# Kernel tuning notes

Measured on AMD Instinct MI355X. Metric: run time of the kernel, lower is better.

Reference implementation:

```python
import jax, jax.numpy as jnp
import numpy as np

E = 384        # number of edges
HID = 128      # hidden_dim
NH = 8         # num_heads
DH = HID // NH # head_dim = 16
NR = 64        # num_radial
CUTOFF = 10.0
AIN = 2 * DH + NR + 1  # attention MLP input dim = 97


def _xavier(key, fan_in, fan_out):
    a = np.sqrt(6.0 / (fan_in + fan_out))
    return jax.random.uniform(key, (fan_in, fan_out), jnp.float32, -a, a)


def setup_inputs() -> dict:
    key = jax.random.key(0)
    ks = jax.random.split(key, 16)
    return {
        "edge_features": jax.random.normal(ks[0], (E, HID), jnp.float32),
        "edge_coords": jax.random.normal(ks[1], (E, 3), jnp.float32),
        "edge_mask": jnp.zeros((E, E), jnp.float32),  # 0 = connected
        "wq": _xavier(ks[2], HID, HID),
        "wk": _xavier(ks[3], HID, HID),
        "wv": _xavier(ks[4], HID, HID),
        "rbf_centers": jnp.linspace(0.0, CUTOFF, NR).astype(jnp.float32),
        "rbf_widths": jnp.full((NR,), 0.5, jnp.float32),
        "a_w1": _xavier(ks[5], AIN, HID), "a_b1": jnp.zeros((HID,), jnp.float32),
        "a_w2": _xavier(ks[6], HID, HID), "a_b2": jnp.zeros((HID,), jnp.float32),
        "a_w3": _xavier(ks[7], HID, NH),  "a_b3": jnp.zeros((NH,), jnp.float32),
        "g_w1": _xavier(ks[8], DH, HID),  "g_b1": jnp.zeros((HID,), jnp.float32),
        "g_w2": _xavier(ks[9], HID, 1),   "g_b2": jnp.zeros((1,), jnp.float32),
        "wo": _xavier(ks[10], HID, HID),  "bo": jnp.zeros((HID,), jnp.float32),
        "ln_g": jnp.ones((HID,), jnp.float32),
        "ln_b": jnp.zeros((HID,), jnp.float32),
        "edge_index": jax.random.randint(ks[11], (2, E), 0, E, jnp.int64) if jax.config.jax_enable_x64 else jax.random.randint(ks[11], (2, E), 0, E, jnp.int32),
    }


def reference(edge_features, edge_coords, edge_mask,
              wq, wk, wv, rbf_centers, rbf_widths,
              a_w1, a_b1, a_w2, a_b2, a_w3, a_b3,
              g_w1, g_b1, g_w2, g_b2, wo, bo, ln_g, ln_b,
              edge_index):
    silu = jax.nn.silu
    n = edge_features.shape[0]

    q = (edge_features @ wq).reshape(n, NH, DH)
    k = (edge_features @ wk).reshape(n, NH, DH)
    v = (edge_features @ wv).reshape(n, NH, DH)

    # pairwise geometry [E, E, ...]
    coord_diff = edge_coords[:, None, :] - edge_coords[None, :, :]
    dist = jnp.linalg.norm(coord_diff, axis=-1) + 1e-8
    dist = jnp.clip(dist, 1e-8, 1e8)
    dot = jnp.clip(jnp.sum(edge_coords[:, None, :] * edge_coords[None, :, :], -1),
                   -1e8, 1e8)
    d = dist[..., None]                               # [E, E, 1]
    rbf = jnp.exp(-rbf_widths * (d - rbf_centers) ** 2) * (d <= CUTOFF).astype(jnp.float32)

    feats = []
    coords = edge_coords
    for h in range(NH):  # structural loop over fixed num_heads
        qh = jnp.broadcast_to(q[:, h, None, :], (n, n, DH))
        kh = jnp.broadcast_to(k[None, :, h, :], (n, n, DH))
        ai = jnp.concatenate([qh, kh, rbf, dot[..., None]], -1)  # [E, E, 97]
        x = silu(ai @ a_w1 + a_b1)
        x = silu(x @ a_w2 + a_b2)
        scores = (x @ a_w3 + a_b3)[:, :, h] + edge_mask
        scores = jnp.clip(scores, -1e9, 1e9)
        attn = jax.nn.softmax(scores, axis=-1)
        attn = jnp.nan_to_num(attn, nan=0.0, posinf=1.0, neginf=0.0)
        vh = v[:, h, :]
        feats.append(attn @ vh)
        # coord gate from v_head of the query edge, broadcast over keys
        gates = jax.nn.sigmoid(silu(vh @ g_w1 + g_b1) @ g_w2 + g_b2)  # [E, 1]
        coords = coords + jnp.einsum('ij,ijc->ic', attn * gates, coord_diff) / NH

    upd = jnp.concatenate(feats, -1)             # [E, hidden]
    y = edge_features + upd @ wo + bo            # residual + out_proj
    mu = jnp.mean(y, -1, keepdims=True)
    var = jnp.var(y, -1, keepdims=True)
    out_f = (y - mu) / jnp.sqrt(var + 1e-5) * ln_g + ln_b
    return out_f, coords
```

## Files before the change

kernel.cpp:

```cpp
#include <hip/hip_runtime.h>
#include <hip/hip_bf16.h>

#define N 384
#define HIDN 128
#define NHD 8
#define DHD 16
#define NRB 64
#define CUTF 10.0f

#define WS_V 0
#define WS_QPB (WS_V + N*HIDN)
#define WS_KPB (WS_QPB + N*NHD*HIDN/2)
#define WS_GATE (WS_KPB + N*NHD*HIDN/2)
#define WS_UPD (WS_GATE + N*NHD)
#define WS_SCORES (WS_UPD + N*HIDN)
#define WS_W2BF (WS_SCORES + NHD*N*N)

typedef short bf16x8 __attribute__((ext_vector_type(8)));
typedef float floatx4 __attribute__((ext_vector_type(4)));
#define MFMA16(a, b, c) __builtin_amdgcn_mfma_f32_16x16x32_bf16(a, b, c, 0, 0, 0)

__device__ __forceinline__ float siluf(float x) { return x / (1.0f + __expf(-x)); }
__device__ __forceinline__ float silu_fast(float x) {
    return x * __builtin_amdgcn_rcpf(1.0f + __expf(-x));
}
__device__ __forceinline__ short f2bf(float f) {
    unsigned int b = __float_as_uint(f);
    unsigned int r = (b + 0x7fffu + ((b >> 16) & 1u)) >> 16;
    return (short)r;
}
__device__ __forceinline__ float bf2f(short s) {
    return __uint_as_float(((unsigned int)(unsigned short)s) << 16);
}
__device__ __forceinline__ unsigned int cvt_pk_bf16(float lo, float hi) {
    unsigned int r;
    asm("v_cvt_pk_bf16_f32 %0, %1, %2" : "=v"(r) : "v"(lo), "v"(hi));
    return r;
}
__device__ __forceinline__ float wave_sum(float v) {
    for (int o = 32; o; o >>= 1) v += __shfl_down(v, o, 64);
    return v;
}

__global__ __launch_bounds__(128) void k_pre(const float* __restrict__ ef,
    const float* __restrict__ wq, const float* __restrict__ wk, const float* __restrict__ wv,
    const float* __restrict__ aw1, const float* __restrict__ aw2,
    const float* __restrict__ gw1, const float* __restrict__ gb1,
    const float* __restrict__ gw2, const float* __restrict__ gb2,
    float* __restrict__ v, unsigned short* __restrict__ Qpb,
    unsigned short* __restrict__ Kpb, float* __restrict__ gates,
    unsigned short* __restrict__ w2bf) {
    __shared__ float sE[HIDN], sQ[HIDN], sK[HIDN], sV[HIDN];
    __shared__ float sG[NHD][2];
    int i = blockIdx.x, t = threadIdx.x;
    if (i < HIDN) w2bf[(size_t)i * HIDN + t] = (unsigned short)f2bf(aw2[t * HIDN + i]);
    sE[t] = ef[i * HIDN + t];
    __syncthreads();
    float aq = 0.f, ak = 0.f, av = 0.f;
#pragma unroll 8
    for (int c = 0; c < HIDN; c++) {
        float e = sE[c];
        aq += e * wq[c * HIDN + t];
        ak += e * wk[c * HIDN + t];
        av += e * wv[c * HIDN + t];
    }
    v[i * HIDN + t] = av;
    sQ[t] = aq; sK[t] = ak; sV[t] = av;
    __syncthreads();
    for (int h = 0; h < NHD; h++) {
        float accq = 0.f, acck = 0.f;
#pragma unroll
        for (int d = 0; d < DHD; d++) {
            accq += sQ[h * DHD + d] * aw1[d * HIDN + t];
            acck += sK[h * DHD + d] * aw1[(DHD + d) * HIDN + t];
        }
        Qpb[((size_t)h * N + i) * HIDN + t] = (unsigned short)f2bf(accq);
        Kpb[((size_t)h * N + i) * HIDN + t] = (unsigned short)f2bf(acck);
        float tt = gb1[t];
#pragma unroll
        for (int d = 0; d < DHD; d++) tt += sV[h * DHD + d] * gw1[d * HIDN + t];
        float contrib = siluf(tt) * gw2[t];
        float s = wave_sum(contrib);
        if ((t & 63) == 0) sG[h][t >> 6] = s;
    }
    __syncthreads();
    if (t < NHD)
        gates[i * NHD + t] = 1.0f / (1.0f + __expf(-(sG[t][0] + sG[t][1] + gb2[0])));
}

#define OFF_W2T  0
#define OFF_QPB  32768
#define OFF_SDD  34816
#define OFF_RBF  34944
#define OFF_R    39040
#define OFF_B2W3 47488
#define SMEM_SZ  52096

__global__ __launch_bounds__(512, 4) void k_scores_mfma(
    const float* __restrict__ coords, const float* __restrict__ mask,
    const float* __restrict__ centers, const float* __restrict__ widths,
    const float* __restrict__ aw1, const float* __restrict__ ab1,
    const float* __restrict__ ab2,
    const float* __restrict__ aw3, const float* __restrict__ ab3,
    const unsigned short* __restrict__ Qpb, const unsigned short* __restrict__ Kpb,
    const unsigned short* __restrict__ w2bf,
    float* __restrict__ scores) {
    __shared__ __align__(16) char smem[SMEM_SZ];
    const int t = threadIdx.x;
    const int lane = t & 63;
    const int w = t >> 6;
    const int l15 = lane & 15;
    const int quad = lane >> 4;
    const int i = blockIdx.y;
    const int jb = blockIdx.x * 96;

    {
        const uint4* src = (const uint4*)w2bf;
        for (int idx = t; idx < 2048; idx += 512) {
            int row = idx >> 4, slot = idx & 15;
            *(uint4*)(smem + OFF_W2T + row * 256 + ((slot * 16) ^ ((row & 7) << 4))) = src[idx];
        }
    }
    if (t < 128)
        ((uint4*)(smem + OFF_QPB))[t] = ((const uint4*)(Qpb + (size_t)i * NHD * HIDN))[t];
    for (int idx = t; idx < HIDN * NHD; idx += 512) {
        int c = idx >> 3, h = idx & 7;
        unsigned int lo = (unsigned short)f2bf(ab2[c]);
        unsigned int hi = (unsigned short)f2bf(aw3[c * NHD + h]);
        *(unsigned int*)(smem + OFF_B2W3 + (c * 9 + h) * 4) = (hi << 16) | lo;
    }
    const int c0 = w * 16 + l15;
    bf16x8 BW1[2];
#pragma unroll
    for (int ks = 0; ks < 2; ks++) {
        bf16x8 a;
#pragma unroll
        for (int e = 0; e < 8; e++) {
            int r = ks * 32 + quad * 8 + e;
            a[e] = f2bf(aw1[(32 + r) * HIDN + c0]);
        }
        BW1[ks] = a;
    }
    const float b1v = ab1[c0];
    const float w1dv = aw1[96 * HIDN + c0];
    const float ab3v = ab3[w];
    const float cr = centers[lane], rwd = widths[lane];
    const float cix = coords[i * 3], ciy = coords[i * 3 + 1], ciz = coords[i * 3 + 2];
    __syncthreads();

    for (int ch = 0; ch < 3; ch++) {
        const int j0 = jb + ch * 32;
        {
#pragma unroll
            for (int p = 0; p < 4; p++) {
                int j = w + p * 8;
                int jj = j0 + j;
                float jx = coords[jj * 3], jy = coords[jj * 3 + 1], jz = coords[jj * 3 + 2];
                float dx = cix - jx, dy = ciy - jy, dz = ciz - jz;
                float dist = sqrtf(dx * dx + dy * dy + dz * dz) + 1e-8f;
                dist = fminf(fmaxf(dist, 1e-8f), 1e8f);
                float dd = dist - cr;
                float val = (dist <= CUTF) ? __expf(-rwd * dd * dd) : 0.0f;
                *(short*)(smem + OFF_RBF + j * 128 + ((lane * 2) ^ ((j & 7) << 4))) = f2bf(val);
            }
            if (t < 32) {
                int jj = j0 + t;
                float jx = coords[jj * 3], jy = coords[jj * 3 + 1], jz = coords[jj * 3 + 2];
                float dot = fminf(fmaxf(cix * jx + ciy * jy + ciz * jz, -1e8f), 1e8f);
                *(float*)(smem + OFF_SDD + t * 4) = dot;
            }
        }
        __syncthreads();
#pragma unroll
        for (int jt = 0; jt < 2; jt++) {
            {
                int jl = jt * 16 + l15;
                int sw = (jl & 7) << 4;
                bf16x8 ra0 = *(const bf16x8*)(smem + OFF_RBF + jl * 128 + ((quad * 16) ^ sw));
                bf16x8 ra1 = *(const bf16x8*)(smem + OFF_RBF + jl * 128 + ((64 + quad * 16) ^ sw));
                floatx4 acc;
#pragma unroll
                for (int r = 0; r < 4; r++) {
                    float dotv = *(const float*)(smem + OFF_SDD + (jt * 16 + quad * 4 + r) * 4);
                    acc[r] = b1v + dotv * w1dv;
                }
                acc = MFMA16(ra0, BW1[0], acc);
                acc = MFMA16(ra1, BW1[1], acc);
#pragma unroll
                for (int r = 0; r < 4; r++)
                    *(float*)(smem + OFF_R + (quad * 4 + r) * 528 + c0 * 4) = acc[r];
            }
            __syncthreads();
            {
                const int jr = j0 + jt * 16 + l15;
                bf16x8 A[4];
#pragma unroll
                for (int f = 0; f < 4; f++) {
                    const int c8 = f * 32 + quad * 8;
                    bf16x8 kp = *(const bf16x8*)(Kpb + ((size_t)w * N + jr) * HIDN + c8);
                    bf16x8 qp = *(const bf16x8*)(smem + OFF_QPB + (w * HIDN + c8) * 2);
                    const char* rbase = smem + OFF_R + l15 * 528 + c8 * 4;
                    float4 r0 = *(const float4*)(rbase);
                    float4 r1 = *(const float4*)(rbase + 16);
                    float xs[8] = {r0.x, r0.y, r0.z, r0.w, r1.x, r1.y, r1.z, r1.w};
                    union { unsigned int u[4]; bf16x8 v; } uu;
#pragma unroll
                    for (int e2 = 0; e2 < 4; e2++) {
                        float xa = silu_fast(bf2f(kp[2 * e2])     + bf2f(qp[2 * e2])     + xs[2 * e2]);
                        float xb = silu_fast(bf2f(kp[2 * e2 + 1]) + bf2f(qp[2 * e2 + 1]) + xs[2 * e2 + 1]);
                        uu.u[e2] = cvt_pk_bf16(xa, xb);
                    }
                    A[f] = uu.v;
                }
                float part[4] = {0.f, 0.f, 0.f, 0.f};
#pragma unroll 2
                for (int ct = 0; ct < 8; ct++) {
                    const int rw2 = ct * 16 + l15;
                    const char* wb = smem + OFF_W2T + rw2 * 256;
                    const int sw = (rw2 & 7) << 4;
                    bf16x8 b0 = *(const bf16x8*)(wb + ((quad * 16) ^ sw));
                    bf16x8 b1 = *(const bf16x8*)(wb + ((64 + quad * 16) ^ sw));
                    bf16x8 b2 = *(const bf16x8*)(wb + ((128 + quad * 16) ^ sw));
                    bf16x8 b3 = *(const bf16x8*)(wb + ((192 + quad * 16) ^ sw));
                    unsigned int pk = *(const unsigned int*)(smem + OFF_B2W3 + (rw2 * 9 + w) * 4);
                    float bb = bf2f((short)(pk & 0xffffu));
                    float ww = bf2f((short)(pk >> 16));
                    floatx4 acc = {bb, bb, bb, bb};
                    acc = MFMA16(A[0], b0, acc);
                    acc = MFMA16(A[1], b1, acc);
                    acc = MFMA16(A[2], b2, acc);
                    acc = MFMA16(A[3], b3, acc);
#pragma unroll
                    for (int r = 0; r < 4; r++)
                        part[r] += silu_fast(acc[r]) * ww;
                }
#pragma unroll
                for (int off = 1; off < 16; off <<= 1) {
#pragma unroll
                    for (int r = 0; r < 4; r++)
                        part[r] += __shfl_xor(part[r], off, 64);
                }
                if (l15 == 0) {
                    const int jo = j0 + jt * 16 + quad * 4;
                    float4 mv = *(const float4*)(mask + (size_t)i * N + jo);
                    float4 sv;
                    sv.x = fminf(fmaxf(part[0] + ab3v + mv.x, -1e9f), 1e9f);
                    sv.y = fminf(fmaxf(part[1] + ab3v + mv.y, -1e9f), 1e9f);
                    sv.z = fminf(fmaxf(part[2] + ab3v + mv.z, -1e9f), 1e9f);
                    sv.w = fminf(fmaxf(part[3] + ab3v + mv.w, -1e9f), 1e9f);
                    *(float4*)(scores + ((size_t)w * N + i) * N + jo) = sv;
                }
            }
            __syncthreads();
        }
    }
}

__global__ __launch_bounds__(256) void k_attn2(
    const float* __restrict__ scores, const float* __restrict__ v,
    const float* __restrict__ gates, const float* __restrict__ coords,
    const float* __restrict__ ef, const float* __restrict__ wo,
    const float* __restrict__ bo, const float* __restrict__ lng,
    const float* __restrict__ lnb, float* __restrict__ out) {
    __shared__ float sA[4][N];
    __shared__ float sCrd[N * 3];
    __shared__ float sC[NHD][3];
    __shared__ float sUpd[HIDN];
    __shared__ float sR2[2];
    int i = blockIdx.x, t = threadIdx.x, w = t >> 6, lane = t & 63;
    for (int idx = t; idx < N * 3; idx += 256) sCrd[idx] = coords[idx];
    float cix = coords[i * 3], ciy = coords[i * 3 + 1], ciz = coords[i * 3 + 2];
    __syncthreads();
    for (int hh = 0; hh < 2; hh++) {
        int h = hh * 4 + w;
        const float* srow = scores + ((size_t)h * N + i) * N;
        float s[6];
#pragma unroll
        for (int p = 0; p < 6; p++) s[p] = srow[lane + 64 * p];
        float m = s[0];
#pragma unroll
        for (int p = 1; p < 6; p++) m = fmaxf(m, s[p]);
        for (int off = 1; off < 64; off <<= 1) m = fmaxf(m, __shfl_xor(m, off, 64));
        float e[6], sum = 0.f;
#pragma unroll
        for (int p = 0; p < 6; p++) { e[p] = __expf(s[p] - m); sum += e[p]; }
        for (int off = 1; off < 64; off <<= 1) sum += __shfl_xor(sum, off, 64);
        float inv = 1.0f / sum;
#pragma unroll
        for (int p = 0; p < 6; p++) sA[w][lane + 64 * p] = e[p] * inv;
        __syncthreads();
        int d4 = lane & 3, grp = lane >> 2;
        float4 f4 = {0.f, 0.f, 0.f, 0.f};
        for (int j = grp; j < N; j += 16) {
            float a = sA[w][j];
            float4 vv = *(const float4*)(v + j * HIDN + h * DHD + d4 * 4);
            f4.x += a * vv.x; f4.y += a * vv.y; f4.z += a * vv.z; f4.w += a * vv.w;
        }
#pragma unroll
        for (int off = 4; off < 64; off <<= 1) {
            f4.x += __shfl_xor(f4.x, off, 64);
            f4.y += __shfl_xor(f4.y, off, 64);
            f4.z += __shfl_xor(f4.z, off, 64);
            f4.w += __shfl_xor(f4.w, off, 64);
        }
        if (lane < 4) *(float4*)(&sUpd[h * DHD + lane * 4]) = f4;
        float cx = 0.f, cy = 0.f, cz = 0.f;
#pragma unroll
        for (int p = 0; p < 6; p++) {
            int j = lane + 64 * p;
            float a = sA[w][j];
            cx += a * (cix - sCrd[j * 3]);
            cy += a * (ciy - sCrd[j * 3 + 1]);
            cz += a * (ciz - sCrd[j * 3 + 2]);
        }
        for (int off = 1; off < 64; off <<= 1) {
            cx += __shfl_xor(cx, off, 64);
            cy += __shfl_xor(cy, off, 64);
            cz += __shfl_xor(cz, off, 64);
        }
        if (lane == 0) {
            float g = gates[i * NHD + h] * (1.0f / NHD);
            sC[h][0] = g * cx; sC[h][1] = g * cy; sC[h][2] = g * cz;
        }
        __syncthreads();
    }
    if (t < 3) {
        float acc = coords[i * 3 + t];
#pragma unroll
        for (int h = 0; h < NHD; h++) acc += sC[h][t];
        out[N * HIDN + i * 3 + t] = acc;
    }
    int c = t & 127;
    float y = ef[i * HIDN + c] + bo[c];
#pragma unroll 8
    for (int cp = 0; cp < HIDN; cp++) y += sUpd[cp] * wo[cp * HIDN + c];
    float ssum = wave_sum(y);
    if (t < 128 && (t & 63) == 0) sR2[t >> 6] = ssum;
    __syncthreads();
    float mu = (sR2[0] + sR2[1]) * (1.0f / HIDN);
    __syncthreads();
    float dv = y - mu;
    float s2 = wave_sum(dv * dv);
    if (t < 128 && (t & 63) == 0) sR2[t >> 6] = s2;
    __syncthreads();
    float var = (sR2[0] + sR2[1]) * (1.0f / HIDN);
    if (t < 128) out[i * HIDN + c] = dv * rsqrtf(var + 1e-5f) * lng[c] + lnb[c];
}

extern "C" void kernel_launch(void* const* d_in, const int* in_sizes, int n_in,
                              void* d_out, int out_size, void* d_ws, size_t ws_size,
                              hipStream_t stream) {
    const float* ef      = (const float*)d_in[0];
    const float* coords  = (const float*)d_in[1];
    const float* mask    = (const float*)d_in[2];
    const float* wq      = (const float*)d_in[3];
    const float* wk      = (const float*)d_in[4];
    const float* wv      = (const float*)d_in[5];
    const float* centers = (const float*)d_in[6];
    const float* widths  = (const float*)d_in[7];
    const float* aw1     = (const float*)d_in[8];
    const float* ab1     = (const float*)d_in[9];
    const float* aw2     = (const float*)d_in[10];
    const float* ab2     = (const float*)d_in[11];
    const float* aw3     = (const float*)d_in[12];
    const float* ab3     = (const float*)d_in[13];
    const float* gw1     = (const float*)d_in[14];
    const float* gb1     = (const float*)d_in[15];
    const float* gw2     = (const float*)d_in[16];
    const float* gb2     = (const float*)d_in[17];
    const float* wo      = (const float*)d_in[18];
    const float* bo      = (const float*)d_in[19];
    const float* lng     = (const float*)d_in[20];
    const float* lnb     = (const float*)d_in[21];
    float* ws = (float*)d_ws;
    float* v      = ws + WS_V;
    unsigned short* Qpb = (unsigned short*)(ws + WS_QPB);
    unsigned short* Kpb = (unsigned short*)(ws + WS_KPB);
    float* gates  = ws + WS_GATE;
    float* scores = ws + WS_SCORES;
    unsigned short* w2bf = (unsigned short*)(ws + WS_W2BF);
    float* out = (float*)d_out;

    k_pre<<<N, 128, 0, stream>>>(ef, wq, wk, wv, aw1, aw2, gw1, gb1, gw2, gb2, v, Qpb, Kpb, gates, w2bf);
    k_scores_mfma<<<dim3(4, N), 512, 0, stream>>>(
        coords, mask, centers, widths, aw1, ab1, ab2, aw3, ab3, Qpb, Kpb, w2bf, scores);
    k_attn2<<<N, 256, 0, stream>>>(scores, v, gates, coords, ef, wo, bo, lng, lnb, out);
}
```

Baseline: 253.4 us.

## Software-pipeline RBF computation, store first-layer result as bf16, split out-proj across threads

Result: no change. 255.2 us (+0.7%).

```diff
diff --git a/kernel.cpp b/kernel.cpp
--- a/kernel.cpp
+++ b/kernel.cpp
@@ -93,8 +93,9 @@
 #define OFF_SDD  34816
 #define OFF_RBF  34944
 #define OFF_R    39040
-#define OFF_B2W3 47488
-#define SMEM_SZ  52096
+#define OFF_B2   47744
+#define OFF_W3T  48256
+#define SMEM_SZ  52352
 
 __global__ __launch_bounds__(512, 4) void k_scores_mfma(
     const float* __restrict__ coords, const float* __restrict__ mask,
@@ -121,13 +122,13 @@
             *(uint4*)(smem + OFF_W2T + row * 256 + ((slot * 16) ^ ((row & 7) << 4))) = src[idx];
         }
     }
-    if (t < 128)
+    if (t < 128) {
         ((uint4*)(smem + OFF_QPB))[t] = ((const uint4*)(Qpb + (size_t)i * NHD * HIDN))[t];
+        *(float*)(smem + OFF_B2 + t * 4) = ab2[t];
+    }
     for (int idx = t; idx < HIDN * NHD; idx += 512) {
-        int c = idx >> 3, h = idx & 7;
-        unsigned int lo = (unsigned short)f2bf(ab2[c]);
-        unsigned int hi = (unsigned short)f2bf(aw3[c * NHD + h]);
-        *(unsigned int*)(smem + OFF_B2W3 + (c * 9 + h) * 4) = (hi << 16) | lo;
+        int h = idx >> 7, c = idx & 127;
+        *(float*)(smem + OFF_W3T + (h * 128 + c) * 4) = aw3[c * NHD + h];
     }
     const int c0 = w * 16 + l15;
     bf16x8 BW1[2];
@@ -146,15 +147,56 @@
     const float ab3v = ab3[w];
     const float cr = centers[lane], rwd = widths[lane];
     const float cix = coords[i * 3], ciy = coords[i * 3 + 1], ciz = coords[i * 3 + 2];
+
+    {
+#pragma unroll
+        for (int p = 0; p < 4; p++) {
+            int j = w + p * 8;
+            int jj = jb + j;
+            float jx = coords[jj * 3], jy = coords[jj * 3 + 1], jz = coords[jj * 3 + 2];
+            float dx = cix - jx, dy = ciy - jy, dz = ciz - jz;
+            float dist = sqrtf(dx * dx + dy * dy + dz * dz) + 1e-8f;
+            dist = fminf(fmaxf(dist, 1e-8f), 1e8f);
+            float dd = dist - cr;
+            float val = (dist <= CUTF) ? __expf(-rwd * dd * dd) : 0.0f;
+            *(short*)(smem + OFF_RBF + j * 128 + ((lane * 2) ^ ((j & 7) << 4))) = f2bf(val);
+        }
+        if (t < 32) {
+            int jj = jb + t;
+            float jx = coords[jj * 3], jy = coords[jj * 3 + 1], jz = coords[jj * 3 + 2];
+            float dot = fminf(fmaxf(cix * jx + ciy * jy + ciz * jz, -1e8f), 1e8f);
+            *(float*)(smem + OFF_SDD + t * 4) = dot;
+        }
+    }
     __syncthreads();
 
     for (int ch = 0; ch < 3; ch++) {
         const int j0 = jb + ch * 32;
-        {
+#pragma unroll
+        for (int jt = 0; jt < 2; jt++) {
+            int jl = jt * 16 + l15;
+            int sw = (jl & 7) << 4;
+            bf16x8 ra0 = *(const bf16x8*)(smem + OFF_RBF + jl * 128 + ((quad * 16) ^ sw));
+            bf16x8 ra1 = *(const bf16x8*)(smem + OFF_RBF + jl * 128 + ((64 + quad * 16) ^ sw));
+            floatx4 acc;
+#pragma unroll
+            for (int r = 0; r < 4; r++) {
+                float dotv = *(const float*)(smem + OFF_SDD + (jt * 16 + quad * 4 + r) * 4);
+                acc[r] = b1v + dotv * w1dv;
+            }
+            acc = MFMA16(ra0, BW1[0], acc);
+            acc = MFMA16(ra1, BW1[1], acc);
+#pragma unroll
+            for (int r = 0; r < 4; r++)
+                *(short*)(smem + OFF_R + (jt * 16 + quad * 4 + r) * 272 + c0 * 2) = f2bf(acc[r]);
+        }
+        __syncthreads();
+        if (ch < 2) {
+            const int j0n = j0 + 32;
 #pragma unroll
             for (int p = 0; p < 4; p++) {
                 int j = w + p * 8;
-                int jj = j0 + j;
+                int jj = j0n + j;
                 float jx = coords[jj * 3], jy = coords[jj * 3 + 1], jz = coords[jj * 3 + 2];
                 float dx = cix - jx, dy = ciy - jy, dz = ciz - jz;
                 float dist = sqrtf(dx * dx + dy * dy + dz * dz) + 1e-8f;
@@ -164,95 +206,70 @@
                 *(short*)(smem + OFF_RBF + j * 128 + ((lane * 2) ^ ((j & 7) << 4))) = f2bf(val);
             }
             if (t < 32) {
-                int jj = j0 + t;
+                int jj = j0n + t;
                 float jx = coords[jj * 3], jy = coords[jj * 3 + 1], jz = coords[jj * 3 + 2];
                 float dot = fminf(fmaxf(cix * jx + ciy * jy + ciz * jz, -1e8f), 1e8f);
                 *(float*)(smem + OFF_SDD + t * 4) = dot;
             }
         }
+#pragma unroll
+        for (int jt = 0; jt < 2; jt++) {
+            const int jl = jt * 16 + l15;
+            bf16x8 A[4];
+#pragma unroll
+            for (int f = 0; f < 4; f++) {
+                const int c8 = f * 32 + quad * 8;
+                bf16x8 kp = *(const bf16x8*)(Kpb + ((size_t)w * N + j0 + jl) * HIDN + c8);
+                bf16x8 qp = *(const bf16x8*)(smem + OFF_QPB + (w * HIDN + c8) * 2);
+                bf16x8 rr = *(const bf16x8*)(smem + OFF_R + (jt * 16 + l15) * 272 + c8 * 2);
+                union { unsigned int u[4]; bf16x8 v; } uu;
+#pragma unroll
+                for (int e2 = 0; e2 < 4; e2++) {
+                    float xa = silu_fast(bf2f(kp[2 * e2])     + bf2f(qp[2 * e2])     + bf2f(rr[2 * e2]));
+                    float xb = silu_fast(bf2f(kp[2 * e2 + 1]) + bf2f(qp[2 * e2 + 1]) + bf2f(rr[2 * e2 + 1]));
+                    uu.u[e2] = cvt_pk_bf16(xa, xb);
+                }
+                A[f] = uu.v;
+            }
+            float part[4] = {0.f, 0.f, 0.f, 0.f};
+#pragma unroll 2
+            for (int ct = 0; ct < 8; ct++) {
+                const int rw2 = ct * 16 + l15;
+                const char* wb = smem + OFF_W2T + rw2 * 256;
+                const int sw = (rw2 & 7) << 4;
+                bf16x8 b0 = *(const bf16x8*)(wb + ((quad * 16) ^ sw));
+                bf16x8 b1 = *(const bf16x8*)(wb + ((64 + quad * 16) ^ sw));
+                bf16x8 b2 = *(const bf16x8*)(wb + ((128 + quad * 16) ^ sw));
+                bf16x8 b3 = *(const bf16x8*)(wb + ((192 + quad * 16) ^ sw));
+                float bb = *(const float*)(smem + OFF_B2 + rw2 * 4);
+                float ww = *(const float*)(smem + OFF_W3T + (w * 128 + rw2) * 4);
+                floatx4 acc = {bb, bb, bb, bb};
+                acc = MFMA16(A[0], b0, acc);
+                acc = MFMA16(A[1], b1, acc);
+                acc = MFMA16(A[2], b2, acc);
+                acc = MFMA16(A[3], b3, acc);
+#pragma unroll
+                for (int r = 0; r < 4; r++)
+                    part[r] += silu_fast(acc[r]) * ww;
+            }
+#pragma unroll
+            for (int off = 1; off < 16; off <<= 1) {
+#pragma unroll
+                for (int r = 0; r < 4; r++)
+                    part[r] += __shfl_xor(part[r], off, 64);
+            }
+            if (l15 == 0) {
+                const int jo = j0 + jt * 16 + quad * 4;
+                float4 mv = *(const float4*)(mask + (size_t)i * N + jo);
+                float4 sv;
+                sv.x = fminf(fmaxf(part[0] + ab3v + mv.x, -1e9f), 1e9f);
+                sv.y = fminf(fmaxf(part[1] + ab3v + mv.y, -1e9f), 1e9f);
+                sv.z = fminf(fmaxf(part[2] + ab3v + mv.z, -1e9f), 1e9f);
+                sv.w = fminf(fmaxf(part[3] + ab3v + mv.w, -1e9f), 1e9f);
+                *(float4*)(scores + ((size_t)w * N + i) * N + jo) = sv;
+            }
+        }
         __syncthreads();
-#pragma unroll
-        for (int jt = 0; jt < 2; jt++) {
-            {
-                int jl = jt * 16 + l15;
-                int sw = (jl & 7) << 4;
-                bf16x8 ra0 = *(const bf16x8*)(smem + OFF_RBF + jl * 128 + ((quad * 16) ^ sw));
-                bf16x8 ra1 = *(const bf16x8*)(smem + OFF_RBF + jl * 128 + ((64 + quad * 16) ^ sw));
-                floatx4 acc;
-#pragma unroll
-                for (int r = 0; r < 4; r++) {
-                    float dotv = *(const float*)(smem + OFF_SDD + (jt * 16 + quad * 4 + r) * 4);
-                    acc[r] = b1v + dotv * w1dv;
-                }
-                acc = MFMA16(ra0, BW1[0], acc);
-                acc = MFMA16(ra1, BW1[1], acc);
-#pragma unroll
-                for (int r = 0; r < 4; r++)
-                    *(float*)(smem + OFF_R + (quad * 4 + r) * 528 + c0 * 4) = acc[r];
-            }
-            __syncthreads();
-            {
-                const int jr = j0 + jt * 16 + l15;
-                bf16x8 A[4];
-#pragma unroll
-                for (int f = 0; f < 4; f++) {
-                    const int c8 = f * 32 + quad * 8;
-                    bf16x8 kp = *(const bf16x8*)(Kpb + ((size_t)w * N + jr) * HIDN + c8);
-                    bf16x8 qp = *(const bf16x8*)(smem + OFF_QPB + (w * HIDN + c8) * 2);
-                    const char* rbase = smem + OFF_R + l15 * 528 + c8 * 4;
-                    float4 r0 = *(const float4*)(rbase);
-                    float4 r1 = *(const float4*)(rbase + 16);
-                    float xs[8] = {r0.x, r0.y, r0.z, r0.w, r1.x, r1.y, r1.z, r1.w};
-                    union { unsigned int u[4]; bf16x8 v; } uu;
-#pragma unroll
-                    for (int e2 = 0; e2 < 4; e2++) {
-                        float xa = silu_fast(bf2f(kp[2 * e2])     + bf2f(qp[2 * e2])     + xs[2 * e2]);
-                        float xb = silu_fast(bf2f(kp[2 * e2 + 1]) + bf2f(qp[2 * e2 + 1]) + xs[2 * e2 + 1]);
-                        uu.u[e2] = cvt_pk_bf16(xa, xb);
-                    }
-                    A[f] = uu.v;
-                }
-                float part[4] = {0.f, 0.f, 0.f, 0.f};
-#pragma unroll 2
-                for (int ct = 0; ct < 8; ct++) {
-                    const int rw2 = ct * 16 + l15;
-                    const char* wb = smem + OFF_W2T + rw2 * 256;
-                    const int sw = (rw2 & 7) << 4;
-                    bf16x8 b0 = *(const bf16x8*)(wb + ((quad * 16) ^ sw));
-                    bf16x8 b1 = *(const bf16x8*)(wb + ((64 + quad * 16) ^ sw));
-                    bf16x8 b2 = *(const bf16x8*)(wb + ((128 + quad * 16) ^ sw));
-                    bf16x8 b3 = *(const bf16x8*)(wb + ((192 + quad * 16) ^ sw));
-                    unsigned int pk = *(const unsigned int*)(smem + OFF_B2W3 + (rw2 * 9 + w) * 4);
-                    float bb = bf2f((short)(pk & 0xffffu));
-                    float ww = bf2f((short)(pk >> 16));
-                    floatx4 acc = {bb, bb, bb, bb};
-                    acc = MFMA16(A[0], b0, acc);
-                    acc = MFMA16(A[1], b1, acc);
-                    acc = MFMA16(A[2], b2, acc);
-                    acc = MFMA16(A[3], b3, acc);
-#pragma unroll
-                    for (int r = 0; r < 4; r++)
-                        part[r] += silu_fast(acc[r]) * ww;
-                }
-#pragma unroll
-                for (int off = 1; off < 16; off <<= 1) {
-#pragma unroll
-                    for (int r = 0; r < 4; r++)
-                        part[r] += __shfl_xor(part[r], off, 64);
-                }
-                if (l15 == 0) {
-                    const int jo = j0 + jt * 16 + quad * 4;
-                    float4 mv = *(const float4*)(mask + (size_t)i * N + jo);
-                    float4 sv;
-                    sv.x = fminf(fmaxf(part[0] + ab3v + mv.x, -1e9f), 1e9f);
-                    sv.y = fminf(fmaxf(part[1] + ab3v + mv.y, -1e9f), 1e9f);
-                    sv.z = fminf(fmaxf(part[2] + ab3v + mv.z, -1e9f), 1e9f);
-                    sv.w = fminf(fmaxf(part[3] + ab3v + mv.w, -1e9f), 1e9f);
-                    *(float4*)(scores + ((size_t)w * N + i) * N + jo) = sv;
-                }
-            }
-            __syncthreads();
-        }
     }
 }
 
@@ -266,6 +283,7 @@
     __shared__ float sCrd[N * 3];
     __shared__ float sC[NHD][3];
     __shared__ float sUpd[HIDN];
+    __shared__ float sY[HIDN];
     __shared__ float sR2[2];
     int i = blockIdx.x, t = threadIdx.x, w = t >> 6, lane = t & 63;
     for (int idx = t; idx < N * 3; idx += 256) sCrd[idx] = coords[idx];
@@ -330,10 +348,16 @@
         for (int h = 0; h < NHD; h++) acc += sC[h][t];
         out[N * HIDN + i * 3 + t] = acc;
     }
-    int c = t & 127;
-    float y = ef[i * HIDN + c] + bo[c];
+    int c = t & 127, g = t >> 7;
+    float y = g ? 0.f : (ef[i * HIDN + c] + bo[c]);
 #pragma unroll 8
-    for (int cp = 0; cp < HIDN; cp++) y += sUpd[cp] * wo[cp * HIDN + c];
+    for (int cp = 0; cp < 64; cp++) {
+        int cc = g * 64 + cp;
+        y += sUpd[cc] * wo[cc * HIDN + c];
+    }
+    if (g) sY[c] = y;
+    __syncthreads();
+    if (!g) y += sY[c];
     float ssum = wave_sum(y);
     if (t < 128 && (t & 63) == 0) sR2[t >> 6] = ssum;
     __syncthreads();
```

## Use 512-thread attention blocks with one wave per head and fp32 b2/w3

Applied to the files above, without the earlier changes.

Measured after the change: 249.2 us. Within noise of the previous version (-1.6%).

```diff
diff --git a/kernel.cpp b/kernel.cpp
--- a/kernel.cpp
+++ b/kernel.cpp
@@ -93,7 +93,8 @@
 #define OFF_SDD  34816
 #define OFF_RBF  34944
 #define OFF_R    39040
-#define OFF_B2W3 47488
+#define OFF_B2   47488
+#define OFF_W3T  48000
 #define SMEM_SZ  52096
 
 __global__ __launch_bounds__(512, 4) void k_scores_mfma(
@@ -121,13 +122,13 @@
             *(uint4*)(smem + OFF_W2T + row * 256 + ((slot * 16) ^ ((row & 7) << 4))) = src[idx];
         }
     }
-    if (t < 128)
+    if (t < 128) {
         ((uint4*)(smem + OFF_QPB))[t] = ((const uint4*)(Qpb + (size_t)i * NHD * HIDN))[t];
+        *(float*)(smem + OFF_B2 + t * 4) = ab2[t];
+    }
     for (int idx = t; idx < HIDN * NHD; idx += 512) {
-        int c = idx >> 3, h = idx & 7;
-        unsigned int lo = (unsigned short)f2bf(ab2[c]);
-        unsigned int hi = (unsigned short)f2bf(aw3[c * NHD + h]);
-        *(unsigned int*)(smem + OFF_B2W3 + (c * 9 + h) * 4) = (hi << 16) | lo;
+        int h = idx >> 7, c = idx & 127;
+        *(float*)(smem + OFF_W3T + (h * 128 + c) * 4) = aw3[c * NHD + h];
     }
     const int c0 = w * 16 + l15;
     bf16x8 BW1[2];
@@ -222,9 +223,8 @@
                     bf16x8 b1 = *(const bf16x8*)(wb + ((64 + quad * 16) ^ sw));
                     bf16x8 b2 = *(const bf16x8*)(wb + ((128 + quad * 16) ^ sw));
                     bf16x8 b3 = *(const bf16x8*)(wb + ((192 + quad * 16) ^ sw));
-                    unsigned int pk = *(const unsigned int*)(smem + OFF_B2W3 + (rw2 * 9 + w) * 4);
-                    float bb = bf2f((short)(pk & 0xffffu));
-                    float ww = bf2f((short)(pk >> 16));
+                    float bb = *(const float*)(smem + OFF_B2 + rw2 * 4);
+                    float ww = *(const float*)(smem + OFF_W3T + (w * 128 + rw2) * 4);
                     floatx4 acc = {bb, bb, bb, bb};
                     acc = MFMA16(A[0], b0, acc);
                     acc = MFMA16(A[1], b1, acc);
@@ -256,23 +256,24 @@
     }
 }
 
-__global__ __launch_bounds__(256) void k_attn2(
+__global__ __launch_bounds__(512) void k_attn2(
     const float* __restrict__ scores, const float* __restrict__ v,
     const float* __restrict__ gates, const float* __restrict__ coords,
     const float* __restrict__ ef, const float* __restrict__ wo,
     const float* __restrict__ bo, const float* __restrict__ lng,
     const float* __restrict__ lnb, float* __restrict__ out) {
-    __shared__ float sA[4][N];
+    __shared__ float sA[NHD][N];
     __shared__ float sCrd[N * 3];
     __shared__ float sC[NHD][3];
     __shared__ float sUpd[HIDN];
+    __shared__ float sP[3][HIDN];
     __shared__ float sR2[2];
     int i = blockIdx.x, t = threadIdx.x, w = t >> 6, lane = t & 63;
-    for (int idx = t; idx < N * 3; idx += 256) sCrd[idx] = coords[idx];
+    for (int idx = t; idx < N * 3; idx += 512) sCrd[idx] = coords[idx];
     float cix = coords[i * 3], ciy = coords[i * 3 + 1], ciz = coords[i * 3 + 2];
     __syncthreads();
-    for (int hh = 0; hh < 2; hh++) {
-        int h = hh * 4 + w;
+    {
+        const int h = w;
         const float* srow = scores + ((size_t)h * N + i) * N;
         float s[6];
 #pragma unroll
@@ -288,7 +289,6 @@
         float inv = 1.0f / sum;
 #pragma unroll
         for (int p = 0; p < 6; p++) sA[w][lane + 64 * p] = e[p] * inv;
-        __syncthreads();
         int d4 = lane & 3, grp = lane >> 2;
         float4 f4 = {0.f, 0.f, 0.f, 0.f};
         for (int j = grp; j < N; j += 16) {
@@ -322,18 +322,24 @@
             float g = gates[i * NHD + h] * (1.0f / NHD);
             sC[h][0] = g * cx; sC[h][1] = g * cy; sC[h][2] = g * cz;
         }
-        __syncthreads();
-    }
+    }
+    __syncthreads();
     if (t < 3) {
         float acc = coords[i * 3 + t];
 #pragma unroll
         for (int h = 0; h < NHD; h++) acc += sC[h][t];
         out[N * HIDN + i * 3 + t] = acc;
     }
-    int c = t & 127;
-    float y = ef[i * HIDN + c] + bo[c];
+    int c = t & 127, g = t >> 7;
+    float y = (g == 0) ? (ef[i * HIDN + c] + bo[c]) : 0.f;
 #pragma unroll 8
-    for (int cp = 0; cp < HIDN; cp++) y += sUpd[cp] * wo[cp * HIDN + c];
+    for (int cp = 0; cp < 32; cp++) {
+        int cc = g * 32 + cp;
+        y += sUpd[cc] * wo[cc * HIDN + c];
+    }
+    if (g > 0) sP[g - 1][c] = y;
+    __syncthreads();
+    if (g == 0) y += sP[0][c] + sP[1][c] + sP[2][c];
     float ssum = wave_sum(y);
     if (t < 128 && (t & 63) == 0) sR2[t >> 6] = ssum;
     __syncthreads();
@@ -384,5 +390,5 @@
     k_pre<<<N, 128, 0, stream>>>(ef, wq, wk, wv, aw1, aw2, gw1, gb1, gw2, gb2, v, Qpb, Kpb, gates, w2bf);
     k_scores_mfma<<<dim3(4, N), 512, 0, stream>>>(
         coords, mask, centers, widths, aw1, ab1, ab2, aw3, ab3, Qpb, Kpb, w2bf, scores);
-    k_attn2<<<N, 256, 0, stream>>>(scores, v, gates, coords, ef, wo, bo, lng, lnb, out);
-}
+    k_attn2<<<N, 512, 0, stream>>>(scores, v, gates, coords, ef, wo, bo, lng, lnb, out);
+}
```
